# Optimization experiments

Hardware: AMD Instinct MI355X
Metric: run time of the kernel (lower is better)

The kernel has to match this reference:

```python
import jax, jax.numpy as jnp
import numpy as np

L, LM, B, D, H, DFF = 1024, 1024, 2, 512, 8, 2048
N = 16              # mamba d_state
DI = 2 * D          # mamba d_inner (expand=2)
DCONV = 4
DTR = (D + 15) // 16  # dt_rank = 32
EPS = 1e-5


def _rmsnorm(x, w):
    return x * w / jnp.sqrt(jnp.mean(x * x, -1, keepdims=True) + EPS)


def _layernorm(x, w, b):
    m = jnp.mean(x, -1, keepdims=True)
    v = jnp.mean((x - m) ** 2, -1, keepdims=True)
    return (x - m) / jnp.sqrt(v + EPS) * w + b


def _mha(q, k, v, in_w, in_b, out_w, out_b):
    # q: [Lq,B,D]; k,v: [Lk,B,D]
    Lq, Bb, Dd = q.shape
    Lk = k.shape[0]
    dh = Dd // H
    qp = (q @ in_w[:Dd].T + in_b[:Dd]).reshape(Lq, Bb, H, dh).transpose(1, 2, 0, 3)
    kp = (k @ in_w[Dd:2 * Dd].T + in_b[Dd:2 * Dd]).reshape(Lk, Bb, H, dh).transpose(1, 2, 0, 3)
    vp = (v @ in_w[2 * Dd:].T + in_b[2 * Dd:]).reshape(Lk, Bb, H, dh).transpose(1, 2, 0, 3)
    s = jnp.einsum('bhqd,bhkd->bhqk', qp, kp) * (dh ** -0.5)
    a = jax.nn.softmax(s, axis=-1)
    o = jnp.einsum('bhqk,bhkd->bhqd', a, vp).transpose(2, 0, 1, 3).reshape(Lq, Bb, Dd)
    return o @ out_w.T + out_b, jnp.mean(a, axis=1)  # attn averaged over heads


def _mamba(x, in_w, in_b, conv_w, conv_b, xproj_w, dt_w, dt_b, Alog, Dp, out_w, out_b):
    # x: [B,L,D] -> [B,L,D] selective state-space scan (mamba.py MambaBlock)
    xz = x @ in_w.T + in_b
    xm, z = xz[..., :DI], xz[..., DI:]
    # causal depthwise conv over time (pad left d_conv-1, truncate to L)
    xc = jax.lax.conv_general_dilated(
        xm.transpose(0, 2, 1), conv_w[:, None, :], (1,), [(DCONV - 1, 0)],
        feature_group_count=DI, dimension_numbers=('NCH', 'OIH', 'NCH'))
    xm = jax.nn.silu((xc + conv_b[None, :, None]).transpose(0, 2, 1))  # [B,L,DI]
    dbc = xm @ xproj_w.T
    dt, Bs, Cs = dbc[..., :DTR], dbc[..., DTR:DTR + N], dbc[..., DTR + N:]
    delta = jax.nn.softplus(dt @ dt_w.T + dt_b)           # [B,L,DI]
    A = -jnp.exp(Alog)                                    # [DI,N]
    dA = jnp.exp(delta[..., None] * A)                    # [B,L,DI,N]
    dBx = delta[..., None] * Bs[:, :, None, :] * xm[..., None]

    def step(h, ab):
        a, b = ab
        h = a * h + b
        return h, h

    _, hs = jax.lax.scan(step, jnp.zeros((x.shape[0], DI, N), x.dtype),
                         (dA.transpose(1, 0, 2, 3), dBx.transpose(1, 0, 2, 3)))
    y = jnp.einsum('blin,bln->bli', hs.transpose(1, 0, 2, 3), Cs)
    y = (y + Dp * xm) * jax.nn.silu(z)
    return y @ out_w.T + out_b


def _bimamba(x, ln1_w, ln1_b, ln2_w, ln2_b, f1_w, f1_b, f2_w, f2_b, mp):
    xn = _layernorm(x, ln1_w, ln1_b)
    mf = _mamba(xn, *mp)
    mb = jnp.flip(_mamba(jnp.flip(xn, 1), *mp), 1)
    m = _layernorm(mf + mb, ln2_w, ln2_b)
    ff = jax.nn.gelu(m @ f1_w.T + f1_b, approximate=False) @ f2_w.T + f2_b
    return ff + x


def _forward(tgt, memory,
             sa_in_w, sa_in_b, sa_out_w, sa_out_b,
             ca_in_w, ca_in_b, ca_out_w, ca_out_b,
             n1_w, n2_w, n3_w, n4_w,
             lin1_w, lin1_b, lin2_w, lin2_b,
             ln1_w, ln1_b, ln2_w, ln2_b,
             bff1_w, bff1_b, bff2_w, bff2_b,
             m_in_w, m_in_b, m_conv_w, m_conv_b, m_xproj_w,
             m_dt_w, m_dt_b, m_Alog, m_D, m_out_w, m_out_b):
    t2, _ = _mha(tgt, tgt, tgt, sa_in_w, sa_in_b, sa_out_w, sa_out_b)
    tgt = _rmsnorm(tgt + t2, n1_w)
    t2, attn = _mha(tgt, memory, memory, ca_in_w, ca_in_b, ca_out_w, ca_out_b)
    tgt = _rmsnorm(tgt + t2, n2_w)
    x = tgt.transpose(1, 0, 2)  # l b d -> b l d
    mp = (m_in_w, m_in_b, m_conv_w, m_conv_b, m_xproj_w, m_dt_w, m_dt_b, m_Alog, m_D, m_out_w, m_out_b)
    x = x + _bimamba(x, ln1_w, ln1_b, ln2_w, ln2_b, bff1_w, bff1_b, bff2_w, bff2_b, mp)
    tgt = x.transpose(1, 0, 2)
    tgt = _rmsnorm(tgt, n3_w)
    t2 = jax.nn.relu(tgt @ lin1_w.T + lin1_b) @ lin2_w.T + lin2_b
    tgt = _rmsnorm(tgt + t2, n4_w)
    return tgt, attn


def setup_inputs() -> dict:
    key = jax.random.key(0)
    ks = jax.random.split(key, 24)
    g = lambda i, shape, s=0.02: jax.random.normal(ks[i], shape, dtype=jnp.float32) * s
    inp = {
        'tgt': jax.random.normal(ks[0], (L, B, D), dtype=jnp.float32),
        'memory': jax.random.normal(ks[1], (LM, B, D), dtype=jnp.float32),
        'sa_in_w': g(2, (3 * D, D)), 'sa_in_b': jnp.zeros((3 * D,)),
        'sa_out_w': g(3, (D, D)), 'sa_out_b': jnp.zeros((D,)),
        'ca_in_w': g(4, (3 * D, D)), 'ca_in_b': jnp.zeros((3 * D,)),
        'ca_out_w': g(5, (D, D)), 'ca_out_b': jnp.zeros((D,)),
        'n1_w': jnp.ones((D,)), 'n2_w': jnp.ones((D,)),
        'n3_w': jnp.ones((D,)), 'n4_w': jnp.ones((D,)),
        'lin1_w': g(6, (DFF, D)), 'lin1_b': jnp.zeros((DFF,)),
        'lin2_w': g(7, (D, DFF)), 'lin2_b': jnp.zeros((D,)),
        'ln1_w': jnp.ones((D,)), 'ln1_b': jnp.zeros((D,)),
        'ln2_w': jnp.ones((D,)), 'ln2_b': jnp.zeros((D,)),
        'bff1_w': g(8, (4 * D, D)), 'bff1_b': jnp.zeros((4 * D,)),
        'bff2_w': g(9, (D, 4 * D)), 'bff2_b': jnp.zeros((D,)),
        'm_in_w': g(10, (2 * DI, D)), 'm_in_b': jnp.zeros((2 * DI,)),
        'm_conv_w': g(11, (DI, DCONV), 0.1), 'm_conv_b': jnp.zeros((DI,)),
        'm_xproj_w': g(12, (DTR + 2 * N, DI)),
        'm_dt_w': g(13, (DI, DTR), 0.1), 'm_dt_b': g(14, (DI,), 0.01),
        'm_Alog': jnp.log(jnp.tile(jnp.arange(1, N + 1, dtype=jnp.float32), (DI, 1))),
        'm_D': jnp.ones((DI,)),
        'm_out_w': g(15, (D, DI)), 'm_out_b': jnp.zeros((D,)),
    }
    return inp


def reference(tgt, memory,
              sa_in_w, sa_in_b, sa_out_w, sa_out_b,
              ca_in_w, ca_in_b, ca_out_w, ca_out_b,
              n1_w, n2_w, n3_w, n4_w,
              lin1_w, lin1_b, lin2_w, lin2_b,
              ln1_w, ln1_b, ln2_w, ln2_b,
              bff1_w, bff1_b, bff2_w, bff2_b,
              m_in_w, m_in_b, m_conv_w, m_conv_b, m_xproj_w,
              m_dt_w, m_dt_b, m_Alog, m_D, m_out_w, m_out_b):
    return _forward(tgt, memory,
                    sa_in_w, sa_in_b, sa_out_w, sa_out_b,
                    ca_in_w, ca_in_b, ca_out_w, ca_out_b,
                    n1_w, n2_w, n3_w, n4_w,
                    lin1_w, lin1_b, lin2_w, lin2_b,
                    ln1_w, ln1_b, ln2_w, ln2_b,
                    bff1_w, bff1_b, bff2_w, bff2_b,
                    m_in_w, m_in_b, m_conv_w, m_conv_b, m_xproj_w,
                    m_dt_w, m_dt_b, m_Alog, m_D, m_out_w, m_out_b)
```

## Files before the change

### kernel.cpp

```cpp
#include <hip/hip_runtime.h>
#include <hip/hip_bf16.h>
#include <math.h>

#define L_SEQ 1024
#define BB 2
#define DD 512
#define HH 8
#define DFFN 2048
#define NSTATE 16
#define DI 1024
#define EPSF 1e-5f

typedef __hip_bfloat16 bf16;
typedef __attribute__((ext_vector_type(8))) short short8v;
typedef __attribute__((ext_vector_type(4))) short short4v;
typedef __attribute__((ext_vector_type(4))) float float4v;

__device__ __forceinline__ float bf2f(bf16 v){ return __bfloat162float(v); }
__device__ __forceinline__ bf16 f2bf(float v){ return __float2bfloat16(v); }
__device__ __forceinline__ short f2bfs(float v){
  bf16 t = __float2bfloat16(v);
  short s; __builtin_memcpy(&s, &t, 2);
  return s;
}

__device__ __forceinline__ void powtab(float q1, float* dA){
  float q2=q1*q1, q4=q2*q2, q8=q4*q4;
  dA[0]=q1;       dA[1]=q2;       dA[2]=q2*q1;     dA[3]=q4;
  dA[4]=q4*q1;    dA[5]=q4*q2;    dA[6]=q4*q2*q1;  dA[7]=q8;
  dA[8]=q8*q1;    dA[9]=q8*q2;    dA[10]=q8*q2*q1; dA[11]=q8*q4;
  dA[12]=q8*q4*q1;dA[13]=q8*q4*q2;dA[14]=q8*q4*q2*q1;dA[15]=q8*q8;
}

__global__ void k_detect(const unsigned int* __restrict__ w, int* __restrict__ flag){
  __shared__ int cnt;
  if (threadIdx.x==0) cnt = 0;
  __syncthreads();
  unsigned int x = w[threadIdx.x];
  unsigned int low = x & 0xffffu;
  int e = (int)((low >> 7) & 0xffu);
  int vote = (low==0u) || (e >= 110 && e <= 140);
  atomicAdd(&cnt, vote);
  __syncthreads();
  if (threadIdx.x==0) flag[0] = (cnt >= 128) ? 1 : 0;
}

struct CvtTabF { const void* src[25]; unsigned int off[26]; };
struct CvtTabW { const void* src[12]; unsigned int off[13]; };

__global__ __launch_bounds__(256) void k_cvt(CvtTabF tf, CvtTabW tb,
                                             float* __restrict__ dstF, bf16* __restrict__ dstB,
                                             const int* __restrict__ flag, int totF, int totB){
  const int isbf = flag[0];
  const int tot = totF + totB;
  for (int g = blockIdx.x*256 + threadIdx.x; g < tot; g += gridDim.x*256){
    if (g < totF){
      int k = 0;
      while (tf.off[k+1] <= (unsigned int)g) ++k;
      int e = g - (int)tf.off[k];
      dstF[g] = isbf ? bf2f(((const bf16*)tf.src[k])[e]) : ((const float*)tf.src[k])[e];
    } else {
      int g2 = g - totF;
      int k = 0;
      while (tb.off[k+1] <= (unsigned int)g2) ++k;
      int e = g2 - (int)tb.off[k];
      if (isbf) dstB[g2] = ((const bf16*)tb.src[k])[e];
      else      dstB[g2] = f2bf(((const float*)tb.src[k])[e]);
    }
  }
}

__global__ __launch_bounds__(256) void k_mfma_gemm(
    const void* __restrict__ Ab, int cA, long long sAb, long long sAh, long long sAm,
    const void* __restrict__ Bb, long long sBb, long long sBh, long long sBrow, int cB,
    void* __restrict__ Cb, int outBf, long long sCb, long long sCh, long long sCm,
    const float* __restrict__ bias, float scale, int act, int K, int H)
{
  __shared__ short As[64*40];
  __shared__ short Bs[64*40];
  const int tid = threadIdx.x;
  int bx = blockIdx.x, by = blockIdx.y;
  if (gridDim.z == 1 && (gridDim.y & 7) == 0){
    int gx = gridDim.x;
    int lin = by*gx + bx;
    int xcd = lin & 7, i = lin >> 3;
    by = xcd*(gridDim.y >> 3) + i / gx;
    bx = i % gx;
  }
  const int z = blockIdx.z; const int zb = z / H; const int zh = z % H;
  const int col0 = bx << 6, m0 = by << 6;
  const float* Af = (const float*)Ab;
  const bf16*  Aw = (const bf16*)Ab;
  const long long aoff = zb*sAb + zh*sAh;
  const float* Bf = (const float*)Bb;
  const bf16* Bw = (const bf16*)Bb;
  const long long boff = zb*sBb + zh*sBh;
  float4v acc[4];
  #pragma unroll
  for (int i=0;i<4;++i) acc[i] = (float4v)(0.f);
  const int lane = tid & 63, w = tid >> 6;
  const int lr = lane & 15, quad = lane >> 4;

  for (int k0 = 0; k0 < K; k0 += 32){
    if (cA == 1){
      int row = tid >> 2, k8 = (tid & 3) << 3;
      short8v v = *(const short8v*)&Aw[aoff + (long long)(m0+row)*sAm + k0 + k8];
      *(short8v*)&As[row*40 + k8] = v;
    } else {
      #pragma unroll
      for (int i=0;i<2;++i){
        int g = tid + i*256;
        int row = g >> 3, k4 = (g & 7) << 2;
        float4 v = *(const float4*)&Af[aoff + (long long)(m0+row)*sAm + k0 + k4];
        short4v s4; s4.x=f2bfs(v.x); s4.y=f2bfs(v.y); s4.z=f2bfs(v.z); s4.w=f2bfs(v.w);
        *(short4v*)&As[row*40 + k4] = s4;
      }
    }
    if (cB == 2){
      int row = tid >> 2, k8 = (tid & 3) << 3;
      short8v v = *(const short8v*)&Bw[boff + (long long)(col0+row)*sBrow + k0 + k8];
      *(short8v*)&Bs[row*40 + k8] = v;
    } else {
      #pragma unroll
      for (int i=0;i<2;++i){
        int g = tid + i*256;
        int row = g >> 3, k4 = (g & 7) << 2;
        float4 v = *(const float4*)&Bf[boff + (long long)(col0+row)*sBrow + k0 + k4];
        short4v s4; s4.x=f2bfs(v.x); s4.y=f2bfs(v.y); s4.z=f2bfs(v.z); s4.w=f2bfs(v.w);
        *(short4v*)&Bs[row*40 + k4] = s4;
      }
    }
    __syncthreads();
    short8v a = *(short8v*)&As[(w*16 + lr)*40 + quad*8];
    #pragma unroll
    for (int cb=0; cb<4; ++cb){
      short8v bfr = *(short8v*)&Bs[(cb*16 + lr)*40 + quad*8];
      acc[cb] = __builtin_amdgcn_mfma_f32_16x16x32_bf16(a, bfr, acc[cb], 0, 0, 0);
    }
    __syncthreads();
  }
  #pragma unroll
  for (int cb=0; cb<4; ++cb){
    #pragma unroll
    for (int r=0;r<4;++r){
      int m = m0 + w*16 + quad*4 + r;
      int n = col0 + cb*16 + lr;
      float v = acc[cb][r] * scale;
      if (bias) v += bias[n];
      if (act==1) v = fmaxf(v,0.f);
      else if (act==2) v = 0.5f*v*(1.f + erff(v*0.70710678118654752f));
      else if (act==3) v = fmaxf(v,0.f) + log1pf(__expf(-fabsf(v)));
      if (outBf) ((bf16*)Cb)[zb*sCb + zh*sCh + (long long)m*sCm + n] = f2bf(v);
      else       ((float*)Cb)[zb*sCb + zh*sCh + (long long)m*sCm + n] = v;
    }
  }
}

__global__ __launch_bounds__(256) void k_gemm_skp(
    const void* __restrict__ Ab, int cA, long long sAz, long long sAm,
    const bf16* __restrict__ Bw, long long sBrow,
    float* __restrict__ Cp, long long sCp, long long sCm,
    const float* __restrict__ bias, int K, int KS)
{
  __shared__ short As[64*40];
  __shared__ short Bs[64*40];
  const int tid = threadIdx.x;
  int bx, by, bz;
  {
    int gx = gridDim.x, gy = gridDim.y, gz = gridDim.z;
    int lin = ((int)blockIdx.z*gy + blockIdx.y)*gx + blockIdx.x;
    int xcd = lin & 7, i = lin >> 3;
    bx = i % gx; int rest = i / gx;
    int pair = xcd * ((gy*gz) >> 3) + rest;
    by = pair % gy; bz = pair / gy;
  }
  const int zb = bz / KS, kc = bz % KS;
  const int Kc = K / KS;
  const int col0 = bx << 6, m0 = by << 6;
  const float* Af = (const float*)Ab;
  const bf16*  Aw = (const bf16*)Ab;
  const long long aoff = (long long)zb*sAz;
  float4v acc[4];
  #pragma unroll
  for (int i=0;i<4;++i) acc[i] = (float4v)(0.f);
  const int lane = tid & 63, w = tid >> 6;
  const int lr = lane & 15, quad = lane >> 4;

  const int kbeg = kc*Kc;
  for (int k0 = kbeg; k0 < kbeg + Kc; k0 += 32){
    if (cA == 1){
      int row = tid >> 2, k8 = (tid & 3) << 3;
      *(short8v*)&As[row*40 + k8] =
        *(const short8v*)&Aw[aoff + (long long)(m0+row)*sAm + k0 + k8];
    } else {
      #pragma unroll
      for (int i=0;i<2;++i){
        int g = tid + i*256;
        int row = g >> 3, k4 = (g & 7) << 2;
        float4 v = *(const float4*)&Af[aoff + (long long)(m0+row)*sAm + k0 + k4];
        short4v s4; s4.x=f2bfs(v.x); s4.y=f2bfs(v.y); s4.z=f2bfs(v.z); s4.w=f2bfs(v.w);
        *(short4v*)&As[row*40 + k4] = s4;
      }
    }
    {
      int row = tid >> 2, k8 = (tid & 3) << 3;
      *(short8v*)&Bs[row*40 + k8] =
        *(const short8v*)&Bw[(long long)(col0+row)*sBrow + k0 + k8];
    }
    __syncthreads();
    short8v a = *(short8v*)&As[(w*16 + lr)*40 + quad*8];
    #pragma unroll
    for (int cb=0; cb<4; ++cb){
      short8v bfr = *(short8v*)&Bs[(cb*16 + lr)*40 + quad*8];
      acc[cb] = __builtin_amdgcn_mfma_f32_16x16x32_bf16(a, bfr, acc[cb], 0, 0, 0);
    }
    __syncthreads();
  }
  #pragma unroll
  for (int cb=0; cb<4; ++cb){
    #pragma unroll
    for (int r=0;r<4;++r){
      int m = m0 + w*16 + quad*4 + r;
      int n = col0 + cb*16 + lr;
      float v = acc[cb][r];
      if (kc == 0 && bias) v += bias[n];
      Cp[(long long)bz*sCp + (long long)m*sCm + n] = v;
    }
  }
}

__global__ __launch_bounds__(256) void k_gemm_sk(
    const void* __restrict__ Ab, int cA, long long sAz, long long sAm,
    const bf16* __restrict__ Bw, long long sBrow,
    float* __restrict__ Cb, long long sCz, long long sCm,
    const float* __restrict__ bias, int K, int KS)
{
  __shared__ short As[64*40];
  __shared__ short Bs[64*40];
  const int tid = threadIdx.x;
  int bx, by, bz;
  {
    int gx = gridDim.x, gy = gridDim.y, gz = gridDim.z;
    int lin = ((int)blockIdx.z*gy + blockIdx.y)*gx + blockIdx.x;
    int xcd = lin & 7, i = lin >> 3;
    bx = i % gx; int rest = i / gx;
    int pair = xcd * ((gy*gz) >> 3) + rest;
    by = pair % gy; bz = pair / gy;
  }
  const int zb = bz / KS, kc = bz % KS;
  const int Kc = K / KS;
  const int col0 = bx << 6, m0 = by << 6;
  const bf16*  Aw = (const bf16*)Ab;
  const float* Af = (const float*)Ab;
  const long long aoff = (long long)zb*sAz;
  float4v acc[4];
  #pragma unroll
  for (int i=0;i<4;++i) acc[i] = (float4v)(0.f);
  const int lane = tid & 63, w = tid >> 6;
  const int lr = lane & 15, quad = lane >> 4;

  const int kbeg = kc*Kc;
  for (int k0 = kbeg; k0 < kbeg + Kc; k0 += 32){
    if (cA == 1){
      int row = tid >> 2, k8 = (tid & 3) << 3;
      *(short8v*)&As[row*40 + k8] =
        *(const short8v*)&Aw[aoff + (long long)(m0+row)*sAm + k0 + k8];
    } else {
      #pragma unroll
      for (int i=0;i<2;++i){
        int g = tid + i*256;
        int row = g >> 3, k4 = (g & 7) << 2;
        float4 v = *(const float4*)&Af[aoff + (long long)(m0+row)*sAm + k0 + k4];
        short4v s4; s4.x=f2bfs(v.x); s4.y=f2bfs(v.y); s4.z=f2bfs(v.z); s4.w=f2bfs(v.w);
        *(short4v*)&As[row*40 + k4] = s4;
      }
    }
    {
      int row = tid >> 2, k8 = (tid & 3) << 3;
      *(short8v*)&Bs[row*40 + k8] =
        *(const short8v*)&Bw[(long long)(col0+row)*sBrow + k0 + k8];
    }
    __syncthreads();
    short8v a = *(short8v*)&As[(w*16 + lr)*40 + quad*8];
    #pragma unroll
    for (int cb=0; cb<4; ++cb){
      short8v bfr = *(short8v*)&Bs[(cb*16 + lr)*40 + quad*8];
      acc[cb] = __builtin_amdgcn_mfma_f32_16x16x32_bf16(a, bfr, acc[cb], 0, 0, 0);
    }
    __syncthreads();
  }
  #pragma unroll
  for (int cb=0; cb<4; ++cb){
    #pragma unroll
    for (int r=0;r<4;++r){
      int m = m0 + w*16 + quad*4 + r;
      int n = col0 + cb*16 + lr;
      float v = acc[cb][r];
      if (kc == 0 && bias) v += bias[n];
      atomicAdd(&Cb[(long long)zb*sCz + (long long)m*sCm + n], v);
    }
  }
}

__global__ __launch_bounds__(256) void k_flash2(
    const bf16* __restrict__ Qb, int ldq, int qoff,
    const bf16* __restrict__ Kb, int ldk, int koff,
    const bf16* __restrict__ Vb, int ldv, int voff,
    bf16* __restrict__ Opart, float* __restrict__ Ml, float scale)
{
  __shared__ short Qs[64*40];
  __shared__ short Ks[64*40];
  __shared__ short Vs[64*40];
  __shared__ short Ps[64*40];
  const int tid = threadIdx.x;
  const int q0 = blockIdx.x << 6;
  const int z = blockIdx.y; const int b = z >> 3; const int hoff = (z & 7) << 6;
  const int kc = blockIdx.z;
  const int lane = tid & 63, w = tid >> 6;
  const int lr = lane & 15, quad = lane >> 4;

  #pragma unroll
  for (int i=0;i<2;++i){
    int idx = tid + i*256;
    int row = idx >> 3, d8 = (idx & 7) << 3;
    *(short8v*)&Qs[row*40 + d8] =
      *(const short8v*)&Qb[(size_t)((q0+row)*BB + b)*ldq + qoff + hoff + d8];
  }

  float m_r[4], l_r[4];
  #pragma unroll
  for (int r=0;r<4;++r){ m_r[r] = -1e30f; l_r[r] = 0.f; }
  float4v acc_o[4];
  #pragma unroll
  for (int cb=0;cb<4;++cb) acc_o[cb] = (float4v)(0.f);

  short8v kr[2], vr[2];
  #pragma unroll
  for (int i=0;i<2;++i){
    int idx = tid + i*256;
    int row = kc*128 + (idx >> 3); int d8 = (idx & 7) << 3;
    kr[i] = *(const short8v*)&Kb[(size_t)(row*BB + b)*ldk + koff + hoff + d8];
    vr[i] = *(const short8v*)&Vb[(size_t)(row*BB + b)*ldv + voff + hoff + d8];
  }

  for (int kt=0; kt<2; ++kt){
    __syncthreads();
    #pragma unroll
    for (int i=0;i<2;++i){
      int idx = tid + i*256;
      int row = idx >> 3, d8 = (idx & 7) << 3;
      *(short8v*)&Ks[row*40 + d8] = kr[i];
      int sc = row ^ d8;
      #pragma unroll
      for (int j=0;j<8;++j) Vs[(d8+j)*40 + sc] = vr[i][j];
    }
    if (kt < 1){
      #pragma unroll
      for (int i=0;i<2;++i){
        int idx = tid + i*256;
        int row = kc*128 + 64 + (idx >> 3); int d8 = (idx & 7) << 3;
        kr[i] = *(const short8v*)&Kb[(size_t)(row*BB + b)*ldk + koff + hoff + d8];
        vr[i] = *(const short8v*)&Vb[(size_t)(row*BB + b)*ldv + voff + hoff + d8];
      }
    }
    __syncthreads();
    short8v a0 = *(short8v*)&Qs[(w*16+lr)*40 + quad*8];
    short8v a1 = *(short8v*)&Qs[(w*16+lr)*40 + quad*8 + 32];
    float4v s[4];
    #pragma unroll
    for (int cb=0;cb<4;++cb){
      short8v b0 = *(short8v*)&Ks[(cb*16+lr)*40 + quad*8];
      short8v b1 = *(short8v*)&Ks[(cb*16+lr)*40 + quad*8 + 32];
      float4v t = __builtin_amdgcn_mfma_f32_16x16x32_bf16(a0, b0, (float4v)(0.f), 0,0,0);
      s[cb] = __builtin_amdgcn_mfma_f32_16x16x32_bf16(a1, b1, t, 0,0,0);
    }
    #pragma unroll
    for (int cb=0;cb<4;++cb)
      #pragma unroll
      for (int r=0;r<4;++r) s[cb][r] *= scale;
    float al[4];
    #pragma unroll
    for (int r=0;r<4;++r){
      float mx = fmaxf(fmaxf(s[0][r],s[1][r]),fmaxf(s[2][r],s[3][r]));
      #pragma unroll
      for (int ofs=1; ofs<16; ofs<<=1) mx = fmaxf(mx, __shfl_xor(mx, ofs));
      float mnew = fmaxf(m_r[r], mx);
      al[r] = __expf(m_r[r] - mnew);
      float sum = 0.f;
      #pragma unroll
      for (int cb=0;cb<4;++cb){
        float p = __expf(s[cb][r] - mnew);
        s[cb][r] = p;
        sum += p;
      }
      #pragma unroll
      for (int ofs=1; ofs<16; ofs<<=1) sum += __shfl_xor(sum, ofs);
      l_r[r] = l_r[r]*al[r] + sum;
      m_r[r] = mnew;
    }
    #pragma unroll
    for (int cb=0;cb<4;++cb)
      #pragma unroll
      for (int r=0;r<4;++r){
        acc_o[cb][r] *= al[r];
        Ps[(w*16 + quad*4 + r)*40 + cb*16 + lr] = f2bfs(s[cb][r]);
      }
    __syncthreads();
    short8v p0 = *(short8v*)&Ps[(w*16+lr)*40 + quad*8];
    short8v p1 = *(short8v*)&Ps[(w*16+lr)*40 + quad*8 + 32];
    #pragma unroll
    for (int cb=0;cb<4;++cb){
      int dcol = cb*16 + lr;
      int sw = (dcol >> 3) & 7;
      short8v v0 = *(short8v*)&Vs[dcol*40 + ((quad ^ sw) << 3)];
      short8v v1 = *(short8v*)&Vs[dcol*40 + (((quad+4) ^ sw) << 3)];
      acc_o[cb] = __builtin_amdgcn_mfma_f32_16x16x32_bf16(p0, v0, acc_o[cb], 0,0,0);
      acc_o[cb] = __builtin_amdgcn_mfma_f32_16x16x32_bf16(p1, v1, acc_o[cb], 0,0,0);
    }
  }
  #pragma unroll
  for (int r=0;r<4;++r){
    int row = q0 + w*16 + quad*4 + r;
    size_t obase = ((size_t)(kc*16 + z)*1024 + row)*64;
    #pragma unroll
    for (int cb=0;cb<4;++cb)
      Opart[obase + cb*16 + lr] = f2bf(acc_o[cb][r]);
    if (lr == 0){
      size_t mi = ((size_t)kc*16384 + z*1024 + row)*2;
      Ml[mi] = m_r[r]; Ml[mi+1] = l_r[r];
    }
  }
}

__global__ __launch_bounds__(256) void k_fcomb(const bf16* __restrict__ Opart, const float* __restrict__ Ml,
                                               bf16* __restrict__ O, float* __restrict__ Mfin)
{
  int gid = blockIdx.x*256 + threadIdx.x;
  int row = gid >> 6, d = gid & 63;
  int z = row >> 10, q = row & 1023;
  float m[8], l[8];
  #pragma unroll
  for (int kc=0;kc<8;++kc){
    size_t mi = ((size_t)kc*16384 + row)*2;
    m[kc] = Ml[mi]; l[kc] = Ml[mi+1];
  }
  float ms = -1e30f;
  #pragma unroll
  for (int kc=0;kc<8;++kc) ms = fmaxf(ms, m[kc]);
  float ls = 0.f, o = 0.f;
  #pragma unroll
  for (int kc=0;kc<8;++kc){
    float c = __expf(m[kc]-ms);
    ls += l[kc]*c;
    o  += bf2f(Opart[((size_t)kc*16384 + row)*64 + d]) * c;
  }
  o /= ls;
  int b = z >> 3, hoff = (z & 7) << 6;
  O[((size_t)q*BB + b)*512 + hoff + d] = f2bf(o);
  if (d == 0){ Mfin[(size_t)row*2] = ms; Mfin[(size_t)row*2+1] = ls; }
}

__global__ __launch_bounds__(256) void k_pmean(
    const bf16* __restrict__ Qb, int ldq,
    const bf16* __restrict__ Kb, int ldk,
    const float* __restrict__ Mfin, void* __restrict__ out,
    const int* __restrict__ flag, float scale)
{
  __shared__ short Qs[64*40];
  __shared__ short Ks[64*40];
  const int tid = threadIdx.x;
  const int k0 = blockIdx.x << 6, q0 = blockIdx.y << 6;
  const int b = blockIdx.z;
  const int lane = tid & 63, w = tid >> 6;
  const int lr = lane & 15, quad = lane >> 4;
  float acc[4][4];
  #pragma unroll
  for (int cb=0;cb<4;++cb)
    #pragma unroll
    for (int r=0;r<4;++r) acc[cb][r] = 0.f;

  for (int h=0; h<8; ++h){
    int z = b*8 + h, hoff = h << 6;
    __syncthreads();
    #pragma unroll
    for (int i=0;i<2;++i){
      int idx = tid + i*256;
      int row = idx >> 3, d8 = (idx & 7) << 3;
      *(short8v*)&Qs[row*40 + d8] = *(const short8v*)&Qb[((size_t)(q0+row)*BB + b)*ldq + hoff + d8];
      *(short8v*)&Ks[row*40 + d8] = *(const short8v*)&Kb[((size_t)(k0+row)*BB + b)*ldk + hoff + d8];
    }
    __syncthreads();
    float mm[4], li[4];
    #pragma unroll
    for (int r=0;r<4;++r){
      int qrow = q0 + w*16 + quad*4 + r;
      size_t mi = ((size_t)z*1024 + qrow)*2;
      mm[r] = Mfin[mi]; li[r] = 1.f/Mfin[mi+1];
    }
    short8v a0 = *(short8v*)&Qs[(w*16+lr)*40 + quad*8];
    short8v a1 = *(short8v*)&Qs[(w*16+lr)*40 + quad*8 + 32];
    #pragma unroll
    for (int cb=0;cb<4;++cb){
      short8v b0 = *(short8v*)&Ks[(cb*16+lr)*40 + quad*8];
      short8v b1 = *(short8v*)&Ks[(cb*16+lr)*40 + quad*8 + 32];
      float4v t = __builtin_amdgcn_mfma_f32_16x16x32_bf16(a0, b0, (float4v)(0.f), 0,0,0);
      t = __builtin_amdgcn_mfma_f32_16x16x32_bf16(a1, b1, t, 0,0,0);
      #pragma unroll
      for (int r=0;r<4;++r)
        acc[cb][r] += __expf(t[r]*scale - mm[r]) * li[r];
    }
  }
  #pragma unroll
  for (int cb=0;cb<4;++cb)
    #pragma unroll
    for (int r=0;r<4;++r){
      int q = q0 + w*16 + quad*4 + r;
      int k = k0 + cb*16 + lr;
      float v = acc[cb][r] * 0.125f;
      size_t o = (size_t)(1u<<20) + ((size_t)b<<20) + (size_t)q*1024 + k;
      if (flag[0]) ((bf16*)out)[o] = f2bf(v);
      else         ((float*)out)[o] = v;
    }
}

__global__ __launch_bounds__(256) void k_add_rmsnorm(float* __restrict__ x, const float* __restrict__ tp,
                                                     long long pstr, int KS, const float* __restrict__ w){
  int row = blockIdx.x; size_t base = (size_t)row*DD;
  int tid = threadIdx.x;
  float v0 = x[base+tid], v1 = x[base+tid+256];
  for (int k=0;k<KS;++k){ v0 += tp[k*pstr + base+tid]; v1 += tp[k*pstr + base+tid+256]; }
  __shared__ float red[256];
  red[tid] = v0*v0 + v1*v1; __syncthreads();
  for (int s=128;s>0;s>>=1){ if(tid<s) red[tid]+=red[tid+s]; __syncthreads(); }
  float rms = rsqrtf(red[0]*(1.f/DD) + EPSF);
  x[base+tid]     = v0 * w[tid]     * rms;
  x[base+tid+256] = v1 * w[tid+256] * rms;
}

__global__ __launch_bounds__(256) void k_add_rmsnorm_out(const float* __restrict__ x, const float* __restrict__ tp,
                                                         long long pstr, int KS,
                                                         const float* __restrict__ w, void* __restrict__ out,
                                                         const int* __restrict__ flag){
  int row = blockIdx.x; size_t base = (size_t)row*DD;
  int tid = threadIdx.x;
  float v0 = x[base+tid], v1 = x[base+tid+256];
  for (int k=0;k<KS;++k){ v0 += tp[k*pstr + base+tid]; v1 += tp[k*pstr + base+tid+256]; }
  __shared__ float red[256];
  red[tid] = v0*v0 + v1*v1; __syncthreads();
  for (int s=128;s>0;s>>=1){ if(tid<s) red[tid]+=red[tid+s]; __syncthreads(); }
  float rms = rsqrtf(red[0]*(1.f/DD) + EPSF);
  float o0 = v0 * w[tid]     * rms;
  float o1 = v1 * w[tid+256] * rms;
  if (flag[0]){ ((bf16*)out)[base+tid] = f2bf(o0); ((bf16*)out)[base+tid+256] = f2bf(o1); }
  else        { ((float*)out)[base+tid] = o0;      ((float*)out)[base+tid+256] = o1; }
}

__global__ __launch_bounds__(256) void k_rms_ln(float* __restrict__ tgt, const float* __restrict__ tp,
                                                long long pstr, const float* __restrict__ n2w,
                                                const float* __restrict__ lw, const float* __restrict__ lb,
                                                bf16* __restrict__ xn){
  int r = blockIdx.x;
  int b = r >> 10, l = r & 1023;
  size_t base = ((size_t)l*BB + b)*DD;
  int tid = threadIdx.x;
  float v0 = tgt[base+tid] + tp[base+tid] + tp[pstr + base+tid];
  float v1 = tgt[base+tid+256] + tp[base+tid+256] + tp[pstr + base+tid+256];
  __shared__ float red[256];
  red[tid] = v0*v0 + v1*v1; __syncthreads();
  for (int s=128;s>0;s>>=1){ if(tid<s) red[tid]+=red[tid+s]; __syncthreads(); }
  float rms = rsqrtf(red[0]*(1.f/DD) + EPSF);
  v0 = v0 * n2w[tid]     * rms;
  v1 = v1 * n2w[tid+256] * rms;
  tgt[base+tid] = v0; tgt[base+tid+256] = v1;
  __syncthreads();
  red[tid] = v0 + v1; __syncthreads();
  for (int s=128;s>0;s>>=1){ if(tid<s) red[tid]+=red[tid+s]; __syncthreads(); }
  float mean = red[0]*(1.f/DD);
  __syncthreads();
  red[tid] = v0*v0 + v1*v1; __syncthreads();
  for (int s=128;s>0;s>>=1){ if(tid<s) red[tid]+=red[tid+s]; __syncthreads(); }
  float var = red[0]*(1.f/DD) - mean*mean;
  float rstd = rsqrtf(var + EPSF);
  size_t dst = (size_t)r*DD;
  xn[dst+tid]     = f2bf((v0-mean)*rstd*lw[tid]     + lb[tid]);
  xn[dst+tid+256] = f2bf((v1-mean)*rstd*lw[tid+256] + lb[tid+256]);
}

__global__ __launch_bounds__(256) void k_combine_ln(const float* __restrict__ yp, long long pstr,
                                                    const float* __restrict__ w, const float* __restrict__ bias,
                                                    bf16* __restrict__ mo){
  int r = blockIdx.x; int b = r>>10, l = r&1023;
  size_t rf = (size_t)r*DD;
  size_t rb = ((size_t)(b<<10) + (1023 - l))*DD;
  int tid = threadIdx.x;
  float v0 = yp[rf+tid]     + yp[pstr + rf+tid]     + yp[2*pstr + rb+tid]     + yp[3*pstr + rb+tid];
  float v1 = yp[rf+tid+256] + yp[pstr + rf+tid+256] + yp[2*pstr + rb+tid+256] + yp[3*pstr + rb+tid+256];
  __shared__ float red[256];
  red[tid] = v0 + v1; __syncthreads();
  for (int s=128;s>0;s>>=1){ if(tid<s) red[tid]+=red[tid+s]; __syncthreads(); }
  float mean = red[0]*(1.f/DD);
  __syncthreads();
  red[tid] = v0*v0 + v1*v1; __syncthreads();
  for (int s=128;s>0;s>>=1){ if(tid<s) red[tid]+=red[tid+s]; __syncthreads(); }
  float var = red[0]*(1.f/DD) - mean*mean;
  float rstd = rsqrtf(var + EPSF);
  mo[rf+tid]     = f2bf((v0-mean)*rstd*w[tid]     + bias[tid]);
  mo[rf+tid+256] = f2bf((v1-mean)*rstd*w[tid+256] + bias[tid+256]);
}

__global__ __launch_bounds__(256) void k_bimamba_final(float* __restrict__ tgt, const float* __restrict__ fp,
                                                       long long pstr, const float* __restrict__ w){
  int r = blockIdx.x; int b = r>>10, l = r&1023;
  size_t t = ((size_t)l*BB + b)*DD;
  size_t f = (size_t)r*DD;
  int tid = threadIdx.x;
  float v0 = 2.f*tgt[t+tid], v1 = 2.f*tgt[t+tid+256];
  #pragma unroll
  for (int k=0;k<4;++k){ v0 += fp[k*pstr + f+tid]; v1 += fp[k*pstr + f+tid+256]; }
  __shared__ float red[256];
  red[tid] = v0*v0 + v1*v1; __syncthreads();
  for (int s=128;s>0;s>>=1){ if(tid<s) red[tid]+=red[tid+s]; __syncthreads(); }
  float rms = rsqrtf(red[0]*(1.f/DD) + EPSF);
  tgt[t+tid]     = v0 * w[tid]     * rms;
  tgt[t+tid+256] = v1 * w[tid+256] * rms;
}

__global__ __launch_bounds__(256) void k_conv_silu(const float* __restrict__ xz, const float* __restrict__ cw, const float* __restrict__ cb, bf16* __restrict__ xmc){
  int rev = blockIdx.y;
  int idx = blockIdx.x*256 + threadIdx.x;
  int c = idx & 1023;
  int l = (idx >> 10) & 1023;
  int b = idx >> 20;
  float acc = cb[c];
  float w4[4];
  #pragma unroll
  for (int j=0;j<4;++j) w4[j] = cw[(c<<2)+j];
  #pragma unroll
  for (int j=0;j<4;++j){
    int t = l - 3 + j;
    if (t >= 0){
      int src = rev ? (1023 - t) : t;
      acc = fmaf(w4[j], xz[((size_t)(b<<10) + src)*2048 + c], acc);
    }
  }
  xmc[(size_t)rev*(2u<<20) + idx] = f2bf(acc / (1.f + __expf(-acc)));
}

__global__ __launch_bounds__(256) void k_scan1(
    const bf16* __restrict__ delta_f, const bf16* __restrict__ delta_b,
    const bf16* __restrict__ xmc_f,  const bf16* __restrict__ xmc_b,
    const float* __restrict__ dbc_f,  const float* __restrict__ dbc_b,
    const float* __restrict__ Alog,
    float* __restrict__ hend, float* __restrict__ Sdl)
{
  int ch = blockIdx.x*256 + threadIdx.x;
  int c = blockIdx.y;
  int dir = ch >> 11, b = (ch >> 10) & 1, d = ch & 1023;
  const bf16* delta = dir ? delta_b : delta_f;
  const bf16* xmc   = dir ? xmc_b   : xmc_f;
  const float* dbc  = dir ? dbc_b   : dbc_f;
  float Av[NSTATE]; bool fast = true;
  #pragma unroll
  for (int n=0;n<NSTATE;++n){
    Av[n] = -__expf(Alog[d*NSTATE+n]);
    fast = fast && (fabsf(Av[n] + (float)(n+1)) < 1e-4f*(float)(n+1));
  }
  float h[NSTATE];
  #pragma unroll
  for (int n=0;n<NSTATE;++n) h[n]=0.f;
  float S = 0.f;
  int r0 = b*1024 + c*16;
  for (int t=0;t<16;++t){
    int r = r0 + t;
    float dl = bf2f(delta[((size_t)r<<10) + d]);
    float x  = bf2f(xmc[((size_t)r<<10) + d]);
    const float4* bp = (const float4*)(dbc + (size_t)r*64 + 32);
    float Bv[NSTATE];
    ((float4*)Bv)[0]=bp[0]; ((float4*)Bv)[1]=bp[1]; ((float4*)Bv)[2]=bp[2]; ((float4*)Bv)[3]=bp[3];
    S += dl;
    float dx = dl*x;
    float dA[NSTATE];
    if (fast){ powtab(__expf(-dl), dA); }
    else {
      #pragma unroll
      for (int n=0;n<NSTATE;++n) dA[n] = __expf(dl*Av[n]);
    }
    #pragma unroll
    for (int n=0;n<NSTATE;++n)
      h[n] = fmaf(dA[n], h[n], dx*Bv[n]);
  }
  size_t base = ((size_t)c*4096 + ch)*16;
  #pragma unroll
  for (int n=0;n<NSTATE;++n) hend[base+n] = h[n];
  Sdl[c*4096 + ch] = S;
}

__global__ __launch_bounds__(256) void k_scan_carry(const float* __restrict__ Alog,
                                                    float* __restrict__ hh, const float* __restrict__ Sdl)
{
  int g = blockIdx.x*256 + threadIdx.x;
  int ch = g >> 4, n = g & 15;
  int d = ch & 1023;
  float Av = -__expf(Alog[d*16+n]);
  float h = 0.f;
  for (int c=0;c<64;++c){
    size_t base = ((size_t)c*4096 + ch)*16 + n;
    float he = hh[base];
    hh[base] = h;
    h = fmaf(__expf(Av*Sdl[c*4096+ch]), h, he);
  }
}

__global__ __launch_bounds__(256) void k_scan2(
    const bf16* __restrict__ delta_f, const bf16* __restrict__ delta_b,
    const bf16* __restrict__ xmc_f,  const bf16* __restrict__ xmc_b,
    const float* __restrict__ dbc_f,  const float* __restrict__ dbc_b,
    const float* __restrict__ Alog,   const float* __restrict__ hin,
    const float* __restrict__ xz,     const float* __restrict__ Dp,
    bf16* __restrict__ yo)
{
  int ch = blockIdx.x*256 + threadIdx.x;
  int c = blockIdx.y;
  int dir = ch >> 11, b = (ch >> 10) & 1, d = ch & 1023;
  const bf16* delta = dir ? delta_b : delta_f;
  const bf16* xmc   = dir ? xmc_b   : xmc_f;
  const float* dbc  = dir ? dbc_b   : dbc_f;
  float Av[NSTATE]; bool fast = true;
  #pragma unroll
  for (int n=0;n<NSTATE;++n){
    Av[n] = -__expf(Alog[d*NSTATE+n]);
    fast = fast && (fabsf(Av[n] + (float)(n+1)) < 1e-4f*(float)(n+1));
  }
  float h[NSTATE];
  size_t cbase = ((size_t)c*4096 + ch)*16;
  #pragma unroll
  for (int n=0;n<NSTATE;++n) h[n] = hin[cbase+n];
  float Dd = Dp[d];
  int r0 = b*1024 + c*16;
  for (int t=0;t<16;++t){
    int r = r0 + t;
    int lidx = c*16 + t;
    float dl = bf2f(delta[((size_t)r<<10) + d]);
    float x  = bf2f(xmc[((size_t)r<<10) + d]);
    const float4* bp = (const float4*)(dbc + (size_t)r*64 + 32);
    float Bv[NSTATE], Cv[NSTATE];
    ((float4*)Bv)[0]=bp[0]; ((float4*)Bv)[1]=bp[1]; ((float4*)Bv)[2]=bp[2]; ((float4*)Bv)[3]=bp[3];
    ((float4*)Cv)[0]=bp[4]; ((float4*)Cv)[1]=bp[5]; ((float4*)Cv)[2]=bp[6]; ((float4*)Cv)[3]=bp[7];
    float dx = dl*x;
    float dA[NSTATE];
    if (fast){ powtab(__expf(-dl), dA); }
    else {
      #pragma unroll
      for (int n=0;n<NSTATE;++n) dA[n] = __expf(dl*Av[n]);
    }
    float acc0 = 0.f, acc1 = 0.f;
    #pragma unroll
    for (int n=0;n<NSTATE;n+=2){
      h[n]   = fmaf(dA[n],   h[n],   dx*Bv[n]);
      h[n+1] = fmaf(dA[n+1], h[n+1], dx*Bv[n+1]);
      acc0 = fmaf(h[n],   Cv[n],   acc0);
      acc1 = fmaf(h[n+1], Cv[n+1], acc1);
    }
    float acc = acc0 + acc1;
    int src = dir ? (1023 - lidx) : lidx;
    float zz = xz[((size_t)(b<<10) + src)*2048 + 1024 + d];
    float sg = zz / (1.f + __expf(-zz));
    yo[(size_t)dir*(2u<<20) + ((size_t)r<<10) + d] = f2bf((acc + Dd*x) * sg);
  }
}

extern "C" void kernel_launch(void* const* d_in, const int* in_sizes, int n_in,
                              void* d_out, int out_size, void* d_ws, size_t ws_size,
                              hipStream_t stream)
{
  if (n_in < 37) return;
  static const unsigned int SZ[37] = {
    1048576,1048576,786432,1536,262144,512,786432,1536,262144,512,
    512,512,512,512,1048576,2048,1048576,512,512,512,
    512,512,1048576,2048,1048576,512,1048576,2048,4096,1024,
    65536,32768,1024,16384,1024,524288,512
  };
  static const unsigned char ISW[37] = {
    0,0,1,0,1,0,1,0,1,0, 0,0,0,0,1,0,1,0,0,0,
    0,0,1,0,1,0,1,0,0,0, 1,1,0,0,0,1,0
  };
  const long long MF = 1u<<20;
  if (ws_size < (size_t)(32*MF)*sizeof(float)) return;

  float* ws = (float*)d_ws;
  float* inF = ws;
  bf16*  inB = (bf16*)(ws + 3*MF);
  float* t2    = ws + 7*MF;
  float* mbuf  = ws + 8*MF;
  float* proj  = ws + 9*MF;
  float* big   = ws + 12*MF;
  float* ff1   = ws + 28*MF;

  CvtTabF tf; CvtTabW tb;
  unsigned int fOff[37], bOff[37];
  {
    int nf=0, nb=0; unsigned int of=0, ob=0;
    for (int i=0;i<37;++i){
      if (ISW[i]){ tb.src[nb]=d_in[i]; tb.off[nb]=ob; bOff[i]=ob; ob+=SZ[i]; ++nb; }
      else       { tf.src[nf]=d_in[i]; tf.off[nf]=of; fOff[i]=of; of+=SZ[i]; ++nf; }
    }
    tf.off[25]=of; tb.off[12]=ob;
    int* flag = (int*)(ws + 3*MF - 16);

    #define PF(i) (inF + fOff[i])
    #define PW(i) (inB + bOff[i])

    float* tgt_f = PF(0);
    float* mem_f = PF(1);
    bf16* qkvB   = (bf16*)proj;
    bf16* qB     = (bf16*)proj;
    bf16* kvB    = (bf16*)(proj + 1*MF);
    bf16* attnoB = (bf16*)mbuf;
    bf16* xnB    = (bf16*)t2;
    bf16*  OpartB  = (bf16*)big;
    float* Ml      = big + 4*MF;
    float* Mfin    = big + 4*MF + 262144;
    float* tpart   = big + 5*MF;
    float* xz      = big;
    bf16*  xmc_f   = (bf16*)(big + 4*MF);
    bf16*  xmc_b   = (bf16*)(big + 5*MF);
    bf16*  delta_f = (bf16*)(big + 6*MF);
    bf16*  delta_b = (bf16*)(big + 7*MF);
    float* hend    = big + 8*MF;
    float* Sdl     = big + 12*MF;
    float* dbc_f   = proj;
    float* dbc_b   = proj + 131072;
    float* ffop    = big;
    float* lin2p   = big + 4*MF;
    float* yprojp  = big + 8*MF;
    bf16*  ybf     = (bf16*)ff1;
    bf16*  ff1B    = (bf16*)ff1;
    bf16*  mbufB   = (bf16*)mbuf;

    k_detect<<<1,256,0,stream>>>((const unsigned int*)d_in[0], flag);
    k_cvt<<<4096,256,0,stream>>>(tf, tb, inF, inB, flag, (int)of, (int)ob);

    k_mfma_gemm<<<dim3(24,32,1),256,0,stream>>>(tgt_f,0,0,0,512, PW(2),0,0,512,2, qkvB,1,0,0,1536, PF(3),1.f,0,512,1);
    k_flash2<<<dim3(16,16,8),256,0,stream>>>(qkvB,1536,0, qkvB,1536,512, qkvB,1536,1024, OpartB, Ml, 0.125f);
    k_fcomb<<<4096,256,0,stream>>>(OpartB, Ml, attnoB, Mfin);
    k_gemm_skp<<<dim3(8,32,2),256,0,stream>>>(attnoB,1,0,512, PW(4),512, tpart,MF,512, PF(5), 512, 2);
    k_add_rmsnorm<<<2048,256,0,stream>>>(tgt_f, tpart, MF, 2, PF(10));

    k_mfma_gemm<<<dim3(8,32,1),256,0,stream>>>(tgt_f,0,0,0,512, PW(6),0,0,512,2, qB,1,0,0,512, PF(7),1.f,0,512,1);
    k_mfma_gemm<<<dim3(16,32,1),256,0,stream>>>(mem_f,0,0,0,512, PW(6)+(size_t)512*512,0,0,512,2, kvB,1,0,0,1024, PF(7)+512,1.f,0,512,1);
    k_flash2<<<dim3(16,16,8),256,0,stream>>>(qB,512,0, kvB,1024,0, kvB,1024,512, OpartB, Ml, 0.125f);
    k_fcomb<<<4096,256,0,stream>>>(OpartB, Ml, attnoB, Mfin);
    k_pmean<<<dim3(16,16,2),256,0,stream>>>(qB,512, kvB,1024, Mfin, d_out, flag, 0.125f);
    k_gemm_skp<<<dim3(8,32,2),256,0,stream>>>(attnoB,1,0,512, PW(8),512, tpart,MF,512, PF(9), 512, 2);
    k_rms_ln<<<2048,256,0,stream>>>(tgt_f, tpart, MF, PF(11), PF(18), PF(19), xnB);

    k_mfma_gemm<<<dim3(32,32,1),256,0,stream>>>(xnB,1,0,0,512, PW(26),0,0,512,2, xz,0,0,0,2048, PF(27),1.f,0,512,1);
    k_conv_silu<<<dim3(8192,2),256,0,stream>>>(xz, PF(28), PF(29), xmc_f);
    hipMemsetAsync(dbc_f, 0, (size_t)262144*4, stream);
    k_gemm_sk<<<dim3(1,32,8),256,0,stream>>>(xmc_f,1,2*MF,1024, PW(30),1024, dbc_f,131072,64, nullptr, 1024, 4);
    k_mfma_gemm<<<dim3(16,32,2),256,0,stream>>>(dbc_f,0,131072,0,64, PW(31),0,0,32,2, delta_f,1,2*MF,0,1024, PF(32),1.f,3,32,1);
    k_scan1<<<dim3(16,64),256,0,stream>>>(delta_f,delta_b,xmc_f,xmc_b,dbc_f,dbc_b, PF(33), hend, Sdl);
    k_scan_carry<<<256,256,0,stream>>>(PF(33), hend, Sdl);
    k_scan2<<<dim3(16,64),256,0,stream>>>(delta_f,delta_b,xmc_f,xmc_b,dbc_f,dbc_b, PF(33), hend, xz, PF(34), ybf);
    k_gemm_skp<<<dim3(8,32,4),256,0,stream>>>(ybf,1,2*MF,1024, PW(35),1024, yprojp,MF,512, PF(36), 1024, 2);
    k_combine_ln<<<2048,256,0,stream>>>(yprojp, MF, PF(20), PF(21), mbufB);
    k_mfma_gemm<<<dim3(32,32,1),256,0,stream>>>(mbufB,1,0,0,512, PW(22),0,0,512,2, ff1B,1,0,0,2048, PF(23),1.f,2,512,1);
    k_gemm_skp<<<dim3(8,32,4),256,0,stream>>>(ff1B,1,0,2048, PW(24),2048, ffop,MF,512, PF(25), 2048, 4);
    k_bimamba_final<<<2048,256,0,stream>>>(tgt_f, ffop, MF, PF(12));

    k_mfma_gemm<<<dim3(32,32,1),256,0,stream>>>(tgt_f,0,0,0,512, PW(14),0,0,512,2, ff1B,1,0,0,2048, PF(15),1.f,1,512,1);
    k_gemm_skp<<<dim3(8,32,4),256,0,stream>>>(ff1B,1,0,2048, PW(16),2048, lin2p,MF,512, PF(17), 2048, 4);
    k_add_rmsnorm_out<<<2048,256,0,stream>>>(tgt_f, lin2p, MF, 4, PF(13), d_out, flag);
    #undef PF
    #undef PW
  }
}
```

Before: 555.0 us.

## Use 128-row MFMA GEMM tiles and fold detect and memset into other kernels

Adds a GEMM kernel with 128x64 output tiles, where each wave computes 32 rows, and uses it for the QKV, Mamba in-projection and both FFN up-projections. Each B tile is now reused across more rows and fewer blocks are launched. The dtype-detect kernel is merged into the conversion kernel, with every block recomputing the vote, and the dbc memset moves into the conv/silu kernel, which removes two launches. The cost is fewer blocks, so lower occupancy and less parallelism for the smaller GEMMs.

```diff
diff --git a/kernel.cpp b/kernel.cpp
--- a/kernel.cpp
+++ b/kernel.cpp
@@ -32,26 +32,26 @@
   dA[12]=q8*q4*q1;dA[13]=q8*q4*q2;dA[14]=q8*q4*q2*q1;dA[15]=q8*q8;
 }
 
-__global__ void k_detect(const unsigned int* __restrict__ w, int* __restrict__ flag){
+struct CvtTabF { const void* src[25]; unsigned int off[26]; };
+struct CvtTabW { const void* src[12]; unsigned int off[13]; };
+
+__global__ __launch_bounds__(256) void k_cvt(CvtTabF tf, CvtTabW tb,
+                                             const unsigned int* __restrict__ w0,
+                                             float* __restrict__ dstF, bf16* __restrict__ dstB,
+                                             int* __restrict__ flag, int totF, int totB){
   __shared__ int cnt;
   if (threadIdx.x==0) cnt = 0;
   __syncthreads();
-  unsigned int x = w[threadIdx.x];
-  unsigned int low = x & 0xffffu;
-  int e = (int)((low >> 7) & 0xffu);
-  int vote = (low==0u) || (e >= 110 && e <= 140);
-  atomicAdd(&cnt, vote);
+  {
+    unsigned int x = w0[threadIdx.x];
+    unsigned int low = x & 0xffffu;
+    int e = (int)((low >> 7) & 0xffu);
+    int vote = (low==0u) || (e >= 110 && e <= 140);
+    atomicAdd(&cnt, vote);
+  }
   __syncthreads();
-  if (threadIdx.x==0) flag[0] = (cnt >= 128) ? 1 : 0;
-}
-
-struct CvtTabF { const void* src[25]; unsigned int off[26]; };
-struct CvtTabW { const void* src[12]; unsigned int off[13]; };
-
-__global__ __launch_bounds__(256) void k_cvt(CvtTabF tf, CvtTabW tb,
-                                             float* __restrict__ dstF, bf16* __restrict__ dstB,
-                                             const int* __restrict__ flag, int totF, int totB){
-  const int isbf = flag[0];
+  const int isbf = (cnt >= 128) ? 1 : 0;
+  if (blockIdx.x==0 && threadIdx.x==0) flag[0] = isbf;
   const int tot = totF + totB;
   for (int g = blockIdx.x*256 + threadIdx.x; g < tot; g += gridDim.x*256){
     if (g < totF){
@@ -154,6 +154,88 @@
       else       ((float*)Cb)[zb*sCb + zh*sCh + (long long)m*sCm + n] = v;
     }
   }
+}
+
+__global__ __launch_bounds__(256) void k_gemm_bigA(
+    const void* __restrict__ Ab, int cA, long long sAm,
+    const bf16* __restrict__ Bw, long long sBrow,
+    void* __restrict__ Cb, int outBf, long long sCm,
+    const float* __restrict__ bias, int act, int K)
+{
+  __shared__ short As[128*40];
+  __shared__ short Bs[64*40];
+  const int tid = threadIdx.x;
+  int bx = blockIdx.x, by = blockIdx.y;
+  if ((gridDim.y & 7) == 0){
+    int gx = gridDim.x;
+    int lin = by*gx + bx;
+    int xcd = lin & 7, i = lin >> 3;
+    by = xcd*(gridDim.y >> 3) + i / gx;
+    bx = i % gx;
+  }
+  const int col0 = bx << 6, m0 = by << 7;
+  const float* Af = (const float*)Ab;
+  const bf16*  Aw = (const bf16*)Ab;
+  const int lane = tid & 63, w = tid >> 6;
+  const int lr = lane & 15, quad = lane >> 4;
+  float4v acc[2][4];
+  #pragma unroll
+  for (int mi=0;mi<2;++mi)
+    #pragma unroll
+    for (int cb=0;cb<4;++cb) acc[mi][cb] = (float4v)(0.f);
+
+  for (int k0 = 0; k0 < K; k0 += 32){
+    if (cA == 1){
+      #pragma unroll
+      for (int i=0;i<2;++i){
+        int idx = tid + i*256;
+        int row = idx >> 2, k8 = (idx & 3) << 3;
+        *(short8v*)&As[row*40 + k8] =
+          *(const short8v*)&Aw[(long long)(m0+row)*sAm + k0 + k8];
+      }
+    } else {
+      #pragma unroll
+      for (int i=0;i<4;++i){
+        int g = tid + i*256;
+        int row = g >> 3, k4 = (g & 7) << 2;
+        float4 v = *(const float4*)&Af[(long long)(m0+row)*sAm + k0 + k4];
+        short4v s4; s4.x=f2bfs(v.x); s4.y=f2bfs(v.y); s4.z=f2bfs(v.z); s4.w=f2bfs(v.w);
+        *(short4v*)&As[row*40 + k4] = s4;
+      }
+    }
+    {
+      int row = tid >> 2, k8 = (tid & 3) << 3;
+      *(short8v*)&Bs[row*40 + k8] =
+        *(const short8v*)&Bw[(long long)(col0+row)*sBrow + k0 + k8];
+    }
+    __syncthreads();
+    short8v a[2], bfr[4];
+    #pragma unroll
+    for (int mi=0;mi<2;++mi) a[mi] = *(short8v*)&As[(w*32 + mi*16 + lr)*40 + quad*8];
+    #pragma unroll
+    for (int cb=0;cb<4;++cb) bfr[cb] = *(short8v*)&Bs[(cb*16 + lr)*40 + quad*8];
+    #pragma unroll
+    for (int mi=0;mi<2;++mi)
+      #pragma unroll
+      for (int cb=0;cb<4;++cb)
+        acc[mi][cb] = __builtin_amdgcn_mfma_f32_16x16x32_bf16(a[mi], bfr[cb], acc[mi][cb], 0,0,0);
+    __syncthreads();
+  }
+  #pragma unroll
+  for (int mi=0;mi<2;++mi)
+    #pragma unroll
+    for (int cb=0;cb<4;++cb)
+      #pragma unroll
+      for (int r=0;r<4;++r){
+        int m = m0 + w*32 + mi*16 + quad*4 + r;
+        int n = col0 + cb*16 + lr;
+        float v = acc[mi][cb][r];
+        if (bias) v += bias[n];
+        if (act==1) v = fmaxf(v,0.f);
+        else if (act==2) v = 0.5f*v*(1.f + erff(v*0.70710678118654752f));
+        if (outBf) ((bf16*)Cb)[(long long)m*sCm + n] = f2bf(v);
+        else       ((float*)Cb)[(long long)m*sCm + n] = v;
+      }
 }
 
 __global__ __launch_bounds__(256) void k_gemm_skp(
@@ -625,9 +707,12 @@
   tgt[t+tid+256] = v1 * w[tid+256] * rms;
 }
 
-__global__ __launch_bounds__(256) void k_conv_silu(const float* __restrict__ xz, const float* __restrict__ cw, const float* __restrict__ cb, bf16* __restrict__ xmc){
+__global__ __launch_bounds__(256) void k_conv_silu(const float* __restrict__ xz, const float* __restrict__ cw,
+                                                   const float* __restrict__ cb, bf16* __restrict__ xmc,
+                                                   float* __restrict__ dbcz){
   int rev = blockIdx.y;
   int idx = blockIdx.x*256 + threadIdx.x;
+  if (rev == 0 && blockIdx.x < 1024) dbcz[idx] = 0.f;
   int c = idx & 1023;
   int l = (idx >> 10) & 1023;
   int b = idx >> 20;
@@ -837,10 +922,9 @@
     bf16*  ff1B    = (bf16*)ff1;
     bf16*  mbufB   = (bf16*)mbuf;
 
-    k_detect<<<1,256,0,stream>>>((const unsigned int*)d_in[0], flag);
-    k_cvt<<<4096,256,0,stream>>>(tf, tb, inF, inB, flag, (int)of, (int)ob);
-
-    k_mfma_gemm<<<dim3(24,32,1),256,0,stream>>>(tgt_f,0,0,0,512, PW(2),0,0,512,2, qkvB,1,0,0,1536, PF(3),1.f,0,512,1);
+    k_cvt<<<4096,256,0,stream>>>(tf, tb, (const unsigned int*)d_in[0], inF, inB, flag, (int)of, (int)ob);
+
+    k_gemm_bigA<<<dim3(24,16),256,0,stream>>>(tgt_f,0,512, PW(2),512, qkvB,1,1536, PF(3),0,512);
     k_flash2<<<dim3(16,16,8),256,0,stream>>>(qkvB,1536,0, qkvB,1536,512, qkvB,1536,1024, OpartB, Ml, 0.125f);
     k_fcomb<<<4096,256,0,stream>>>(OpartB, Ml, attnoB, Mfin);
     k_gemm_skp<<<dim3(8,32,2),256,0,stream>>>(attnoB,1,0,512, PW(4),512, tpart,MF,512, PF(5), 512, 2);
@@ -854,9 +938,8 @@
     k_gemm_skp<<<dim3(8,32,2),256,0,stream>>>(attnoB,1,0,512, PW(8),512, tpart,MF,512, PF(9), 512, 2);
     k_rms_ln<<<2048,256,0,stream>>>(tgt_f, tpart, MF, PF(11), PF(18), PF(19), xnB);
 
-    k_mfma_gemm<<<dim3(32,32,1),256,0,stream>>>(xnB,1,0,0,512, PW(26),0,0,512,2, xz,0,0,0,2048, PF(27),1.f,0,512,1);
-    k_conv_silu<<<dim3(8192,2),256,0,stream>>>(xz, PF(28), PF(29), xmc_f);
-    hipMemsetAsync(dbc_f, 0, (size_t)262144*4, stream);
+    k_gemm_bigA<<<dim3(32,16),256,0,stream>>>(xnB,1,512, PW(26),512, xz,0,2048, PF(27),0,512);
+    k_conv_silu<<<dim3(8192,2),256,0,stream>>>(xz, PF(28), PF(29), xmc_f, dbc_f);
     k_gemm_sk<<<dim3(1,32,8),256,0,stream>>>(xmc_f,1,2*MF,1024, PW(30),1024, dbc_f,131072,64, nullptr, 1024, 4);
     k_mfma_gemm<<<dim3(16,32,2),256,0,stream>>>(dbc_f,0,131072,0,64, PW(31),0,0,32,2, delta_f,1,2*MF,0,1024, PF(32),1.f,3,32,1);
     k_scan1<<<dim3(16,64),256,0,stream>>>(delta_f,delta_b,xmc_f,xmc_b,dbc_f,dbc_b, PF(33), hend, Sdl);
@@ -864,11 +947,11 @@
     k_scan2<<<dim3(16,64),256,0,stream>>>(delta_f,delta_b,xmc_f,xmc_b,dbc_f,dbc_b, PF(33), hend, xz, PF(34), ybf);
     k_gemm_skp<<<dim3(8,32,4),256,0,stream>>>(ybf,1,2*MF,1024, PW(35),1024, yprojp,MF,512, PF(36), 1024, 2);
     k_combine_ln<<<2048,256,0,stream>>>(yprojp, MF, PF(20), PF(21), mbufB);
-    k_mfma_gemm<<<dim3(32,32,1),256,0,stream>>>(mbufB,1,0,0,512, PW(22),0,0,512,2, ff1B,1,0,0,2048, PF(23),1.f,2,512,1);
+    k_gemm_bigA<<<dim3(32,16),256,0,stream>>>(mbufB,1,512, PW(22),512, ff1B,1,2048, PF(23),2,512);
     k_gemm_skp<<<dim3(8,32,4),256,0,stream>>>(ff1B,1,0,2048, PW(24),2048, ffop,MF,512, PF(25), 2048, 4);
     k_bimamba_final<<<2048,256,0,stream>>>(tgt_f, ffop, MF, PF(12));
 
-    k_mfma_gemm<<<dim3(32,32,1),256,0,stream>>>(tgt_f,0,0,0,512, PW(14),0,0,512,2, ff1B,1,0,0,2048, PF(15),1.f,1,512,1);
+    k_gemm_bigA<<<dim3(32,16),256,0,stream>>>(tgt_f,0,512, PW(14),512, ff1B,1,2048, PF(15),1,512);
     k_gemm_skp<<<dim3(8,32,4),256,0,stream>>>(ff1B,1,0,2048, PW(16),2048, lin2p,MF,512, PF(17), 2048, 4);
     k_add_rmsnorm_out<<<2048,256,0,stream>>>(tgt_f, lin2p, MF, 4, PF(13), d_out, flag);
     #undef PF
```

After: 582.0 us. +4.9%, slower.
